# Performance work log

Hardware: AMD Instinct MI355X
Metric: run time of the kernel (lower is better)

The kernel has to match this reference:

```python
import jax, jax.numpy as jnp
import numpy as np

N, C, H = 4096, 768, 12
HD = C // H
SCALE = HD ** -0.5


def setup_inputs() -> dict:
    key = jax.random.key(0)
    k1, k2, k3 = jax.random.split(key, 3)
    x = jax.random.normal(k1, (N, C), dtype=jnp.float32)
    w_qkv = jax.random.normal(k2, (C, 3 * C), dtype=jnp.float32) * (C ** -0.5)
    w_proj = jax.random.normal(k3, (C, C), dtype=jnp.float32) * (C ** -0.5)
    b_proj = jnp.zeros((C,), dtype=jnp.float32)
    return {"x": x, "w_qkv": w_qkv, "w_proj": w_proj, "b_proj": b_proj}


def reference(x, w_qkv, w_proj, b_proj):
    n, c = x.shape
    # fused QKV projection (qkv_bias=False): [N, 3C] -> [3, H, N, hd]
    qkv = (x @ w_qkv).reshape(n, 3, H, HD)
    qkv = jnp.transpose(qkv, (1, 2, 0, 3))  # (3, H, N, hd)
    q, k, v = qkv[0], qkv[1], qkv[2]
    # scaled dot-product attention per head: (H, N, N)
    attn = jnp.einsum('hnd,hmd->hnm', q, k) * SCALE
    attn = jax.nn.softmax(attn, axis=-1)
    # attn_drop is identity (rate=0, eval mode)
    out = jnp.einsum('hnm,hmd->hnd', attn, v)          # (H, N, hd)
    out = jnp.transpose(out, (1, 0, 2)).reshape(n, c)  # (N, C)
    # output projection (bias by default in nn.Dense); proj_drop identity
    return out @ w_proj + b_proj
```

## Files before the change

kernel.cpp:

```cpp
#include <hip/hip_runtime.h>

#define N_TOK 4096
#define C_DIM 768
#define H_NUM 12
#define QKV_N 2304

typedef __attribute__((ext_vector_type(8))) short bf16x8;
typedef __attribute__((ext_vector_type(4))) float f32x4;
typedef __attribute__((ext_vector_type(16))) float f32x16;
typedef __attribute__((ext_vector_type(4))) unsigned int u32x4;

static __device__ __forceinline__ unsigned short f2bf(float f) {
  unsigned u = __builtin_bit_cast(unsigned, f);
  u += 0x7FFF + ((u >> 16) & 1);
  return (unsigned short)(u >> 16);
}

static __device__ __forceinline__ float exp2_fast(float x) {
  float r; asm("v_exp_f32 %0, %1" : "=v"(r) : "v"(x)); return r;
}

#define GLOAD_LDS16(g, l)                                                     \
  __builtin_amdgcn_global_load_lds(                                           \
      (const __attribute__((address_space(1))) void*)(g),                     \
      (__attribute__((address_space(3))) void*)(l), 16, 0, 0)

#define Q_SCALE 0.18033688011112042f

__global__ __launch_bounds__(256) void conv_bf16(
    const float* __restrict__ in, unsigned short* __restrict__ out, int n8) {
  const int i = blockIdx.x * 256 + threadIdx.x;
  if (i >= n8) return;
  const float4 a = reinterpret_cast<const float4*>(in)[i * 2];
  const float4 b = reinterpret_cast<const float4*>(in)[i * 2 + 1];
  unsigned short tmp[8] = {f2bf(a.x), f2bf(a.y), f2bf(a.z), f2bf(a.w),
                           f2bf(b.x), f2bf(b.y), f2bf(b.z), f2bf(b.w)};
  reinterpret_cast<bf16x8*>(out)[i] = *reinterpret_cast<bf16x8*>(tmp);
}

__global__ __launch_bounds__(256) void transpose_cvt(
    const float* __restrict__ in, unsigned short* __restrict__ out,
    int K, int N) {
  __shared__ unsigned short T[64][65];
  const int t = threadIdx.x;
  const int k0 = blockIdx.y * 64, n0 = blockIdx.x * 64;
  {
    const int r = t >> 2, qd = t & 3;
#pragma unroll
    for (int i = 0; i < 4; ++i) {
      const int c = qd * 16 + i * 4;
      const float4 v = *reinterpret_cast<const float4*>(
          &in[(size_t)(k0 + r) * N + n0 + c]);
      T[r][c + 0] = f2bf(v.x); T[r][c + 1] = f2bf(v.y);
      T[r][c + 2] = f2bf(v.z); T[r][c + 3] = f2bf(v.w);
    }
  }
  __syncthreads();
#pragma unroll
  for (int i = 0; i < 2; ++i) {
    const int cid = t + i * 256;
    const int rn = cid >> 3, cx = cid & 7;
    unsigned short tmp[8];
#pragma unroll
    for (int j = 0; j < 8; ++j) tmp[j] = T[cx * 8 + j][rn];
    *reinterpret_cast<bf16x8*>(&out[(size_t)(n0 + rn) * K + k0 + cx * 8]) =
        *reinterpret_cast<bf16x8*>(tmp);
  }
}

__global__ __launch_bounds__(256) void gemm_qkv_bf16(
    const unsigned short* __restrict__ A, const unsigned short* __restrict__ Bt,
    unsigned short* __restrict__ qw, unsigned short* __restrict__ kw,
    unsigned short* __restrict__ vw) {
  __shared__ unsigned short As[128 * 32];
  __shared__ unsigned short Bs[128 * 32];
  const int t = threadIdx.x;
  const int lane = t & 63, wid = t >> 6;
  const int lr = lane & 15, lg = lane >> 4;
  const int m_base = blockIdx.y * 128, n_base = blockIdx.x * 128;
  const int wm = (wid >> 1) * 64, wn = (wid & 1) * 64;
  const int c_row = lane >> 2;
  const int c_col = (lane & 3) * 8;

  f32x4 acc[4][4];
#pragma unroll
  for (int mt = 0; mt < 4; ++mt)
#pragma unroll
    for (int nt = 0; nt < 4; ++nt) acc[mt][nt] = (f32x4){0.f, 0.f, 0.f, 0.f};

  for (int kt = 0; kt < 24; ++kt) {
    const int k0 = kt * 32;
    __syncthreads();
#pragma unroll
    for (int i = 0; i < 2; ++i) {
      const int ch = wid * 2 + i;
      GLOAD_LDS16(&A[(size_t)(m_base + ch * 16 + c_row) * 768 + k0 + c_col],
                  &As[ch * 512]);
      GLOAD_LDS16(&Bt[(size_t)(n_base + ch * 16 + c_row) * 768 + k0 + c_col],
                  &Bs[ch * 512]);
    }
    __syncthreads();
    bf16x8 af[4], bfr[4];
#pragma unroll
    for (int mt = 0; mt < 4; ++mt)
      af[mt] = *reinterpret_cast<const bf16x8*>(&As[(wm + mt * 16 + lr) * 32 + lg * 8]);
#pragma unroll
    for (int nt = 0; nt < 4; ++nt)
      bfr[nt] = *reinterpret_cast<const bf16x8*>(&Bs[(wn + nt * 16 + lr) * 32 + lg * 8]);
#pragma unroll
    for (int mt = 0; mt < 4; ++mt)
#pragma unroll
      for (int nt = 0; nt < 4; ++nt)
        acc[mt][nt] = __builtin_amdgcn_mfma_f32_16x16x32_bf16(af[mt], bfr[nt],
                                                              acc[mt][nt], 0, 0, 0);
  }
#pragma unroll
  for (int mt = 0; mt < 4; ++mt)
#pragma unroll
    for (int nt = 0; nt < 4; ++nt)
#pragma unroll
      for (int r = 0; r < 4; ++r) {
        const int m = m_base + wm + mt * 16 + lg * 4 + r;
        const int c = n_base + wn + nt * 16 + lr;
        const float v = acc[mt][nt][r];
        const int which = c / 768;
        const int cc = c - which * 768;
        const int h = cc >> 6, d = cc & 63;
        if (which == 0) {
          qw[((size_t)h * N_TOK + m) * 64 + d] = f2bf(v * Q_SCALE);
        } else if (which == 1) {
          kw[((size_t)h * N_TOK + m) * 64 + d] = f2bf(v);
        } else {
          vw[((size_t)h * 64 + d) * N_TOK + m] = f2bf(v);
        }
      }
}

__global__ __launch_bounds__(256) void gemm_proj_bf16(
    const unsigned short* __restrict__ A, const unsigned short* __restrict__ Bt,
    const float* __restrict__ bias, float* __restrict__ out) {
  __shared__ unsigned short As[128 * 32];
  __shared__ unsigned short Bs[128 * 32];
  const int t = threadIdx.x;
  const int lane = t & 63, wid = t >> 6;
  const int lr = lane & 15, lg = lane >> 4;
  const int m_base = blockIdx.y * 128, n_base = blockIdx.x * 128;
  const int wm = (wid >> 1) * 64, wn = (wid & 1) * 64;
  const int c_row = lane >> 2;
  const int c_col = (lane & 3) * 8;

  f32x4 acc[4][4];
#pragma unroll
  for (int mt = 0; mt < 4; ++mt)
#pragma unroll
    for (int nt = 0; nt < 4; ++nt) acc[mt][nt] = (f32x4){0.f, 0.f, 0.f, 0.f};

  for (int kt = 0; kt < 24; ++kt) {
    const int k0 = kt * 32;
    __syncthreads();
#pragma unroll
    for (int i = 0; i < 2; ++i) {
      const int ch = wid * 2 + i;
      GLOAD_LDS16(&A[(size_t)(m_base + ch * 16 + c_row) * 768 + k0 + c_col],
                  &As[ch * 512]);
      GLOAD_LDS16(&Bt[(size_t)(n_base + ch * 16 + c_row) * 768 + k0 + c_col],
                  &Bs[ch * 512]);
    }
    __syncthreads();
    bf16x8 af[4], bfr[4];
#pragma unroll
    for (int mt = 0; mt < 4; ++mt)
      af[mt] = *reinterpret_cast<const bf16x8*>(&As[(wm + mt * 16 + lr) * 32 + lg * 8]);
#pragma unroll
    for (int nt = 0; nt < 4; ++nt)
      bfr[nt] = *reinterpret_cast<const bf16x8*>(&Bs[(wn + nt * 16 + lr) * 32 + lg * 8]);
#pragma unroll
    for (int mt = 0; mt < 4; ++mt)
#pragma unroll
      for (int nt = 0; nt < 4; ++nt)
        acc[mt][nt] = __builtin_amdgcn_mfma_f32_16x16x32_bf16(af[mt], bfr[nt],
                                                              acc[mt][nt], 0, 0, 0);
  }
#pragma unroll
  for (int nt = 0; nt < 4; ++nt) {
    const int n = n_base + wn + nt * 16 + lr;
    const float bv = bias[n];
#pragma unroll
    for (int mt = 0; mt < 4; ++mt)
#pragma unroll
      for (int r = 0; r < 4; ++r) {
        const int m = m_base + wm + mt * 16 + lg * 4 + r;
        out[(size_t)m * 768 + n] = acc[mt][nt][r] + bv;
      }
  }
}

__global__ __launch_bounds__(256) void attn_kernel(
    const unsigned short* __restrict__ qw, const unsigned short* __restrict__ kw,
    const unsigned short* __restrict__ vw, unsigned short* __restrict__ ow) {
  __shared__ unsigned short smem[18432];
  const int t = threadIdx.x;
  const int lane = t & 63;
  const int wid = t >> 6;
  const int qsub = wid & 1;
  const int kvh = wid >> 1;
  const int q31 = lane & 31;
  const int hi = lane >> 5;
  const int h = blockIdx.y;
  const int q0 = blockIdx.x * 64 + qsub * 32;

  unsigned short* Ks = &smem[kvh * 9216];
  unsigned short* Vs = Ks + 4608;

  const unsigned short* kbase = &kw[(size_t)h * N_TOK * 64];
  const unsigned short* vbase = &vw[(size_t)h * 64 * N_TOK];
  const int kv0 = kvh * 2048;

  bf16x8 qf[4];
#pragma unroll
  for (int ks = 0; ks < 4; ++ks)
    qf[ks] = *reinterpret_cast<const bf16x8*>(
        &qw[((size_t)h * N_TOK + q0 + q31) * 64 + ks * 16 + hi * 8]);

  f32x16 acc0, acc1;
#pragma unroll
  for (int r = 0; r < 16; ++r) { acc0[r] = 0.f; acc1[r] = 0.f; }
  float m_run = -1e30f, l_run = 0.f;

  const int tg = t & 127;
  const int srow = tg >> 3;
  const int sseg = (tg & 7) * 8;

  bf16x8 kst[4], vst[4];
#pragma unroll
  for (int i = 0; i < 4; ++i) {
    const int row = srow + i * 16;
    kst[i] = *reinterpret_cast<const bf16x8*>(&kbase[(size_t)(kv0 + row) * 64 + sseg]);
    vst[i] = *reinterpret_cast<const bf16x8*>(&vbase[(size_t)row * N_TOK + kv0 + sseg]);
  }

  for (int kvt = 0; kvt < 32; ++kvt) {
    const int kv = kv0 + kvt * 64;
    __syncthreads();
#pragma unroll
    for (int i = 0; i < 4; ++i) {
      const int row = srow + i * 16;
      *reinterpret_cast<bf16x8*>(&Ks[row * 72 + sseg]) = kst[i];
      *reinterpret_cast<bf16x8*>(&Vs[row * 72 + sseg]) = vst[i];
    }
    __syncthreads();
    const int kvn = (kvt + 1 < 32) ? kv + 64 : kv0;
#pragma unroll
    for (int i = 0; i < 4; ++i) {
      const int row = srow + i * 16;
      kst[i] = *reinterpret_cast<const bf16x8*>(&kbase[(size_t)(kvn + row) * 64 + sseg]);
      vst[i] = *reinterpret_cast<const bf16x8*>(&vbase[(size_t)row * N_TOK + kvn + sseg]);
    }

#pragma unroll
    for (int ct = 0; ct < 2; ++ct) {
      f32x16 s;
#pragma unroll
      for (int r = 0; r < 16; ++r) s[r] = 0.f;
#pragma unroll
      for (int ks = 0; ks < 4; ++ks) {
        const bf16x8 kf = *reinterpret_cast<const bf16x8*>(
            &Ks[(ct * 32 + q31) * 72 + ks * 16 + hi * 8]);
        s = __builtin_amdgcn_mfma_f32_32x32x16_bf16(kf, qf[ks], s, 0, 0, 0);
      }
      float m8[8];
#pragma unroll
      for (int r = 0; r < 8; ++r) m8[r] = fmaxf(s[r], s[r + 8]);
#pragma unroll
      for (int r = 0; r < 4; ++r) m8[r] = fmaxf(m8[r], m8[r + 4]);
      float pm = fmaxf(fmaxf(m8[0], m8[1]), fmaxf(m8[2], m8[3]));
      pm = fmaxf(pm, __shfl_xor(pm, 32));
      if (!__all(pm <= m_run + 8.f)) {
        const float newm = fmaxf(m_run, pm);
        const float al = exp2_fast(m_run - newm);
        m_run = newm;
        l_run *= al;
#pragma unroll
        for (int r = 0; r < 16; ++r) {
          const float a = __shfl(al, (r & 3) + 8 * (r >> 2) + 4 * hi);
          acc0[r] *= a; acc1[r] *= a;
        }
      }
      float p[16];
#pragma unroll
      for (int r = 0; r < 16; ++r) p[r] = exp2_fast(s[r] - m_run);
      float s8[8];
#pragma unroll
      for (int r = 0; r < 8; ++r) s8[r] = p[r] + p[r + 8];
#pragma unroll
      for (int r = 0; r < 4; ++r) s8[r] = s8[r] + s8[r + 4];
      float rs = (s8[0] + s8[1]) + (s8[2] + s8[3]);
      rs += __shfl_xor(rs, 32);
      l_run += rs;

      unsigned dw[8];
#pragma unroll
      for (int m2 = 0; m2 < 8; ++m2)
        asm("v_cvt_pk_bf16_f32 %0, %1, %2"
            : "=v"(dw[m2]) : "v"(p[2 * m2]), "v"(p[2 * m2 + 1]));
      asm("v_permlane32_swap_b32 %0, %1" : "+v"(dw[0]), "+v"(dw[2]));
      asm("v_permlane32_swap_b32 %0, %1" : "+v"(dw[1]), "+v"(dw[3]));
      asm("v_permlane32_swap_b32 %0, %1" : "+v"(dw[4]), "+v"(dw[6]));
      asm("v_permlane32_swap_b32 %0, %1" : "+v"(dw[5]), "+v"(dw[7]));

#pragma unroll
      for (int ksl = 0; ksl < 2; ++ksl) {
        u32x4 u;
        u.x = dw[ksl * 4 + 0]; u.y = dw[ksl * 4 + 1];
        u.z = dw[ksl * 4 + 2]; u.w = dw[ksl * 4 + 3];
        const bf16x8 pa = __builtin_bit_cast(bf16x8, u);
        const int kg = ct * 2 + ksl;
        const bf16x8 vf0 = *reinterpret_cast<const bf16x8*>(
            &Vs[q31 * 72 + kg * 16 + hi * 8]);
        const bf16x8 vf1 = *reinterpret_cast<const bf16x8*>(
            &Vs[(32 + q31) * 72 + kg * 16 + hi * 8]);
        acc0 = __builtin_amdgcn_mfma_f32_32x32x16_bf16(pa, vf0, acc0, 0, 0, 0);
        acc1 = __builtin_amdgcn_mfma_f32_32x32x16_bf16(pa, vf1, acc1, 0, 0, 0);
      }
    }
  }

  __syncthreads();
  float* ex = reinterpret_cast<float*>(smem) + qsub * 2304;
  if (kvh == 1) {
    float* pdst = ex + lane * 36;
#pragma unroll
    for (int r = 0; r < 16; ++r) { pdst[r] = acc0[r]; pdst[16 + r] = acc1[r]; }
    pdst[32] = m_run;
    pdst[33] = l_run;
  }
  __syncthreads();
  if (kvh == 0) {
    const float* psrc = ex + lane * 36;
    const float mB = psrc[32], lB = psrc[33];
    const float m2 = fmaxf(m_run, mB);
    const float fA = exp2_fast(m_run - m2);
    const float fB = exp2_fast(mB - m2);
    const float linv = 1.0f / (l_run * fA + lB * fB);
    const float gA = fA * linv, gB = fB * linv;
#pragma unroll
    for (int r = 0; r < 16; ++r) {
      const int crow = (r & 3) + 8 * (r >> 2) + 4 * hi;
      const float a = __shfl(gA, crow);
      const float b = __shfl(gB, crow);
      const size_t base = (size_t)(q0 + crow) * C_DIM + h * 64;
      ow[base + q31] = f2bf(acc0[r] * a + psrc[r] * b);
      ow[base + 32 + q31] = f2bf(acc1[r] * a + psrc[16 + r] * b);
    }
  }
}

extern "C" void kernel_launch(void* const* d_in, const int* in_sizes, int n_in,
                              void* d_out, int out_size, void* d_ws, size_t ws_size,
                              hipStream_t stream) {
  (void)in_sizes; (void)n_in; (void)out_size; (void)ws_size;
  const float* x = (const float*)d_in[0];
  const float* w_qkv = (const float*)d_in[1];
  const float* w_proj = (const float*)d_in[2];
  const float* b_proj = (const float*)d_in[3];
  float* out = (float*)d_out;

  const size_t HNd = (size_t)H_NUM * N_TOK * 64;
  unsigned short* qw = (unsigned short*)d_ws;
  unsigned short* kw = qw + HNd;
  unsigned short* vw = kw + HNd;
  unsigned short* xb = vw + HNd;
  unsigned short* ow = xb;
  unsigned short* wT = xb + HNd;
  unsigned short* wqkvT = wT;
  unsigned short* wprojT = wT;

  conv_bf16<<<dim3((N_TOK * C_DIM / 8 + 255) / 256), 256, 0, stream>>>(
      x, xb, N_TOK * C_DIM / 8);
  transpose_cvt<<<dim3(QKV_N / 64, C_DIM / 64), 256, 0, stream>>>(
      w_qkv, wqkvT, C_DIM, QKV_N);
  gemm_qkv_bf16<<<dim3(QKV_N / 128, N_TOK / 128), 256, 0, stream>>>(
      xb, wqkvT, qw, kw, vw);
  transpose_cvt<<<dim3(C_DIM / 64, C_DIM / 64), 256, 0, stream>>>(
      w_proj, wprojT, C_DIM, C_DIM);
  attn_kernel<<<dim3(N_TOK / 64, H_NUM), 256, 0, stream>>>(qw, kw, vw, ow);
  gemm_proj_bf16<<<dim3(C_DIM / 128, N_TOK / 128), 256, 0, stream>>>(
      ow, wprojT, b_proj, out);
}
```

Before: 165.9 us.

## Double-buffer K/V tiles via direct global-to-LDS loads with XOR swizzle

Replaces the register-staged K/V tile copy (global load to VGPRs, then ds_write between two barriers) with global_load_lds into a double-buffered LDS region, so the next tile streams in while the current one is consumed. The padded stride-72 layout becomes a stride-64 layout with an XOR chunk swizzle to avoid bank conflicts, and s_setprio raises wave priority around the MFMA blocks. This removes one barrier per iteration and the staging registers, at the cost of doubling LDS use per block (64 KB), which may lower occupancy.

```diff
diff --git a/kernel.cpp b/kernel.cpp
--- a/kernel.cpp
+++ b/kernel.cpp
@@ -198,7 +198,7 @@
 __global__ __launch_bounds__(256) void attn_kernel(
     const unsigned short* __restrict__ qw, const unsigned short* __restrict__ kw,
     const unsigned short* __restrict__ vw, unsigned short* __restrict__ ow) {
-  __shared__ unsigned short smem[18432];
+  __shared__ unsigned short smem[32768];
   const int t = threadIdx.x;
   const int lane = t & 63;
   const int wid = t >> 6;
@@ -206,16 +206,20 @@
   const int kvh = wid >> 1;
   const int q31 = lane & 31;
   const int hi = lane >> 5;
+  const int q7 = q31 & 7;
   const int h = blockIdx.y;
   const int q0 = blockIdx.x * 64 + qsub * 32;
 
-  unsigned short* Ks = &smem[kvh * 9216];
-  unsigned short* Vs = Ks + 4608;
+  unsigned short* gbase = &smem[kvh * 16384];
 
   const unsigned short* kbase = &kw[(size_t)h * N_TOK * 64];
   const unsigned short* vbase = &vw[(size_t)h * 64 * N_TOK];
   const int kv0 = kvh * 2048;
 
+  const int lr8 = lane >> 3;
+  const int lc8 = lane & 7;
+  const int sck = lc8 ^ lr8;
+
   bf16x8 qf[4];
 #pragma unroll
   for (int ks = 0; ks < 4; ++ks)
@@ -227,47 +231,48 @@
   for (int r = 0; r < 16; ++r) { acc0[r] = 0.f; acc1[r] = 0.f; }
   float m_run = -1e30f, l_run = 0.f;
 
-  const int tg = t & 127;
-  const int srow = tg >> 3;
-  const int sseg = (tg & 7) * 8;
-
-  bf16x8 kst[4], vst[4];
 #pragma unroll
   for (int i = 0; i < 4; ++i) {
-    const int row = srow + i * 16;
-    kst[i] = *reinterpret_cast<const bf16x8*>(&kbase[(size_t)(kv0 + row) * 64 + sseg]);
-    vst[i] = *reinterpret_cast<const bf16x8*>(&vbase[(size_t)row * N_TOK + kv0 + sseg]);
-  }
-
+    const int rk = (qsub * 4 + i) * 8 + lr8;
+    GLOAD_LDS16(&kbase[(size_t)(kv0 + rk) * 64 + sck * 8],
+                &gbase[(qsub * 4 + i) * 512]);
+    GLOAD_LDS16(&vbase[(size_t)rk * N_TOK + kv0 + sck * 8],
+                &gbase[4096 + (qsub * 4 + i) * 512]);
+  }
+
+  int cur = 0;
   for (int kvt = 0; kvt < 32; ++kvt) {
-    const int kv = kv0 + kvt * 64;
-    __syncthreads();
-#pragma unroll
-    for (int i = 0; i < 4; ++i) {
-      const int row = srow + i * 16;
-      *reinterpret_cast<bf16x8*>(&Ks[row * 72 + sseg]) = kst[i];
-      *reinterpret_cast<bf16x8*>(&Vs[row * 72 + sseg]) = vst[i];
-    }
-    __syncthreads();
-    const int kvn = (kvt + 1 < 32) ? kv + 64 : kv0;
-#pragma unroll
-    for (int i = 0; i < 4; ++i) {
-      const int row = srow + i * 16;
-      kst[i] = *reinterpret_cast<const bf16x8*>(&kbase[(size_t)(kvn + row) * 64 + sseg]);
-      vst[i] = *reinterpret_cast<const bf16x8*>(&vbase[(size_t)row * N_TOK + kvn + sseg]);
-    }
+    asm volatile("s_waitcnt vmcnt(0)" ::: "memory");
+    __syncthreads();
+    if (kvt + 1 < 32) {
+      const int kvn = kv0 + (kvt + 1) * 64;
+      unsigned short* nb = gbase + (cur ^ 1) * 8192;
+#pragma unroll
+      for (int i = 0; i < 4; ++i) {
+        const int rk = (qsub * 4 + i) * 8 + lr8;
+        GLOAD_LDS16(&kbase[(size_t)(kvn + rk) * 64 + sck * 8],
+                    &nb[(qsub * 4 + i) * 512]);
+        GLOAD_LDS16(&vbase[(size_t)rk * N_TOK + kvn + sck * 8],
+                    &nb[4096 + (qsub * 4 + i) * 512]);
+      }
+    }
+    const unsigned short* Ks = gbase + cur * 8192;
+    const unsigned short* Vs = Ks + 4096;
+    cur ^= 1;
 
 #pragma unroll
     for (int ct = 0; ct < 2; ++ct) {
       f32x16 s;
 #pragma unroll
       for (int r = 0; r < 16; ++r) s[r] = 0.f;
+      __builtin_amdgcn_s_setprio(1);
 #pragma unroll
       for (int ks = 0; ks < 4; ++ks) {
         const bf16x8 kf = *reinterpret_cast<const bf16x8*>(
-            &Ks[(ct * 32 + q31) * 72 + ks * 16 + hi * 8]);
+            &Ks[(ct * 32 + q31) * 64 + (((ks * 2 + hi) ^ q7) << 3)]);
         s = __builtin_amdgcn_mfma_f32_32x32x16_bf16(kf, qf[ks], s, 0, 0, 0);
       }
+      __builtin_amdgcn_s_setprio(0);
       float m8[8];
 #pragma unroll
       for (int r = 0; r < 8; ++r) m8[r] = fmaxf(s[r], s[r + 8]);
@@ -308,6 +313,7 @@
       asm("v_permlane32_swap_b32 %0, %1" : "+v"(dw[4]), "+v"(dw[6]));
       asm("v_permlane32_swap_b32 %0, %1" : "+v"(dw[5]), "+v"(dw[7]));
 
+      __builtin_amdgcn_s_setprio(1);
 #pragma unroll
       for (int ksl = 0; ksl < 2; ++ksl) {
         u32x4 u;
@@ -315,13 +321,15 @@
         u.z = dw[ksl * 4 + 2]; u.w = dw[ksl * 4 + 3];
         const bf16x8 pa = __builtin_bit_cast(bf16x8, u);
         const int kg = ct * 2 + ksl;
+        const int vchk = ((kg * 2 + hi) ^ q7) << 3;
         const bf16x8 vf0 = *reinterpret_cast<const bf16x8*>(
-            &Vs[q31 * 72 + kg * 16 + hi * 8]);
+            &Vs[q31 * 64 + vchk]);
         const bf16x8 vf1 = *reinterpret_cast<const bf16x8*>(
-            &Vs[(32 + q31) * 72 + kg * 16 + hi * 8]);
+            &Vs[(32 + q31) * 64 + vchk]);
         acc0 = __builtin_amdgcn_mfma_f32_32x32x16_bf16(pa, vf0, acc0, 0, 0, 0);
         acc1 = __builtin_amdgcn_mfma_f32_32x32x16_bf16(pa, vf1, acc1, 0, 0, 0);
       }
+      __builtin_amdgcn_s_setprio(0);
     }
   }
 
```

Measured after the change: 171.8 us. 1.04x slower.
